# Kernel optimization log

Hardware: AMD Instinct MI355X
Metric: run time of the kernel (lower is better)

Reference implementation:

```python
import jax, jax.numpy as jnp
import numpy as np

H = 16       # query heads
KV = 4       # kv heads
BASE = 10000.0


def _rope(seq_len, head_dim, dtype):
    inv_freq = 1.0 / (BASE ** (jnp.arange(0, head_dim, 2, dtype=jnp.float32) / head_dim))
    t = jnp.arange(seq_len, dtype=jnp.float32)
    freqs = jnp.einsum('i,j->ij', t, inv_freq)          # [S, D/2]
    emb = jnp.concatenate([freqs, freqs], axis=-1)      # [S, D]
    return jnp.cos(emb).astype(dtype), jnp.sin(emb).astype(dtype)


def _rotate_half(x):
    x1, x2 = jnp.split(x, 2, axis=-1)
    return jnp.concatenate([-x2, x1], axis=-1)


def setup_inputs() -> dict:
    key = jax.random.key(0)
    ks = jax.random.split(key, 5)
    B, S, E = 2, 2048, 1024
    return {
        'x': jax.random.normal(ks[0], (B, S, E), jnp.float32),
        'wq': jax.random.normal(ks[1], (E, E), jnp.float32) * (E ** -0.5),
        'wk': jax.random.normal(ks[2], (KV * (E // H), E), jnp.float32) * (E ** -0.5),
        'wv': jax.random.normal(ks[3], (KV * (E // H), E), jnp.float32) * (E ** -0.5),
        'wo': jax.random.normal(ks[4], (E, E), jnp.float32) * (E ** -0.5),
    }


def reference(x, wq, wk, wv, wo):
    B, S, E = x.shape
    D = E // H
    G = H // KV  # query heads per kv head
    scale = D ** -0.5

    q = (x @ wq.T).reshape(B, S, H, D).transpose(0, 2, 1, 3)    # [B,H,S,D]
    k = (x @ wk.T).reshape(B, S, KV, D).transpose(0, 2, 1, 3)   # [B,KV,S,D]
    v = (x @ wv.T).reshape(B, S, KV, D).transpose(0, 2, 1, 3)   # [B,KV,S,D]

    cos, sin = _rope(S, D, x.dtype)                              # [S,D] each
    q = q * cos + _rotate_half(q) * sin
    k = k * cos + _rotate_half(k) * sin

    # GQA: group query heads per kv head instead of materializing repeated K/V
    qg = q.reshape(B, KV, G, S, D)
    scores = jnp.einsum('bkgsd,bktd->bkgst', qg, k) * scale      # [B,KV,G,S,S]
    causal = jnp.triu(jnp.ones((S, S), dtype=bool), k=1)
    scores = jnp.where(causal, jnp.finfo(scores.dtype).min, scores)
    attn = jax.nn.softmax(scores, axis=-1)
    out = jnp.einsum('bkgst,bktd->bkgsd', attn, v)               # [B,KV,G,S,D]
    out = out.reshape(B, H, S, D).transpose(0, 2, 1, 3).reshape(B, S, E)
    return out @ wo.T
```

## Files before the change

### kernel.cpp

```cpp
#include <hip/hip_runtime.h>
#include <stdint.h>

typedef unsigned short u16;
typedef __attribute__((ext_vector_type(8))) short s16x8;
typedef __attribute__((ext_vector_type(4))) float f32x4;
typedef __attribute__((ext_vector_type(4))) unsigned short u16x4;


__device__ __forceinline__ u16 f2bf(float f) {
  unsigned u = __float_as_uint(f);
  unsigned r = (u + 0x7fffu + ((u >> 16) & 1u)) >> 16;
  return (u16)r;
}
__device__ __forceinline__ unsigned pack2(float a, float b) {
  return (unsigned)f2bf(a) | ((unsigned)f2bf(b) << 16);
}
__device__ __forceinline__ float exp2fast(float x) {
  return __builtin_amdgcn_exp2f(x);
}

typedef const __attribute__((address_space(1))) unsigned int* gas_ptr;
typedef __attribute__((address_space(3))) unsigned int* las_ptr;

__device__ __forceinline__ void g2l16(const void* g, void* l) {
  __builtin_amdgcn_global_load_lds((gas_ptr)g, (las_ptr)l, 16, 0, 0);
}

__device__ __forceinline__ void cvt4(const float* __restrict__ in, u16* __restrict__ out) {
  const f32x4 v = *(const f32x4*)in;
  u16x4 o;
  o[0] = f2bf(v[0]); o[1] = f2bf(v[1]); o[2] = f2bf(v[2]); o[3] = f2bf(v[3]);
  *(u16x4*)out = o;
}


__global__ void prep_kernel(const float* __restrict__ x,  const float* __restrict__ wq,
                            const float* __restrict__ wk, const float* __restrict__ wv,
                            const float* __restrict__ wo,
                            u16* __restrict__ xb, u16* __restrict__ wcat, u16* __restrict__ wob,
                            float* __restrict__ cosT, float* __restrict__ sinT) {
  const long id = (long)blockIdx.x * 256 + threadIdx.x;
  if (id < 262144) {
    cvt4(wq + id * 4, wcat + id * 4);
  } else if (id < 327680) {
    const long i = id - 262144;
    cvt4(wk + i * 4, wcat + 1048576 + i * 4);
  } else if (id < 393216) {
    const long i = id - 327680;
    cvt4(wv + i * 4, wcat + 1310720 + i * 4);
  } else if (id < 655360) {
    const long i = id - 393216;
    cvt4(wo + i * 4, wob + i * 4);
  } else if (id < 671744) {
    const long t = id - 655360;
#pragma unroll
    for (int u = 0; u < 4; ++u) {
      const long idx = t * 4 + u;
      const int s = (int)(idx >> 5), j = (int)(idx & 31);
      const double invd = exp(-(double)j * 0.2878231366242558);
      const float a = (float)s * (float)invd;
      cosT[idx] = cosf(a);
      sinT[idx] = sinf(a);
    }
  } else {
    const long i = id - 671744;
    cvt4(x + i * 4, xb + i * 4);
  }
}


__global__ __launch_bounds__(256, 2) void gemm_qkv_kernel(
    const u16* __restrict__ A, const u16* __restrict__ W,
    u16* __restrict__ qo, u16* __restrict__ ko, u16* __restrict__ vto,
    const float* __restrict__ cosT, const float* __restrict__ sinT) {
  const int K = 1024;
  __shared__ __align__(16) u16 As[128 * 32];
  __shared__ __align__(16) u16 Bs[128 * 32];
  const int tid = threadIdx.x;
  const int lane = tid & 63;
  const int wave = tid >> 6;
  const int wr = wave >> 1, wc = wave & 1;
  const long arow0 = (long)blockIdx.x * 128;
  const long wrow0 = (long)blockIdx.y * 128;
  const u16* Ab = A + arow0 * K;
  const u16* Wb = W + wrow0 * K;

  f32x4 acc[4][4] = {};

  for (int k0 = 0; k0 < K; k0 += 32) {
    __syncthreads();
#pragma unroll
    for (int i = 0; i < 2; ++i) {
      const int c = wave * 128 + i * 64 + lane;
      const int r = c >> 2, c16 = c & 3;
      g2l16(Ab + (long)r * K + k0 + c16 * 8, (char*)As + (wave * 128 + i * 64) * 16);
      g2l16(Wb + (long)r * K + k0 + c16 * 8, (char*)Bs + (wave * 128 + i * 64) * 16);
    }
    __syncthreads();
    s16x8 af[4], bfr[4];
#pragma unroll
    for (int m = 0; m < 4; ++m) {
      const int row = wr * 64 + m * 16 + (lane & 15);
      af[m] = *(const s16x8*)&As[row * 32 + (lane >> 4) * 8];
    }
#pragma unroll
    for (int n = 0; n < 4; ++n) {
      const int row = wc * 64 + n * 16 + (lane & 15);
      bfr[n] = *(const s16x8*)&Bs[row * 32 + (lane >> 4) * 8];
    }
    __builtin_amdgcn_s_setprio(1);
#pragma unroll
    for (int m = 0; m < 4; ++m)
#pragma unroll
      for (int n = 0; n < 4; ++n)
        acc[m][n] = __builtin_amdgcn_mfma_f32_16x16x32_bf16(af[m], bfr[n], acc[m][n], 0, 0, 0);
    __builtin_amdgcn_s_setprio(0);
  }

  const int colBase = (int)wrow0 + wc * 64;
  const int j0 = lane & 15;
  const float QSCALE = 0.18033688011112042f;

  if (colBase < 1024) {
    const int h2 = colBase >> 6;
#pragma unroll
    for (int m = 0; m < 4; ++m) {
      const int grow = (int)arow0 + wr * 64 + m * 16 + (lane >> 4) * 4;
#pragma unroll
      for (int r = 0; r < 4; ++r) {
        const int row = grow + r;
        const int s = row & 2047, bb = row >> 11;
        const long ob = (((long)(bb * 16 + h2)) * 2048 + s) * 64;
        const float c0 = cosT[s * 32 + j0],      s0 = sinT[s * 32 + j0];
        const float c1 = cosT[s * 32 + 16 + j0], s1 = sinT[s * 32 + 16 + j0];
        qo[ob + j0]      = f2bf((acc[m][0][r] * c0 - acc[m][2][r] * s0) * QSCALE);
        qo[ob + 16 + j0] = f2bf((acc[m][1][r] * c1 - acc[m][3][r] * s1) * QSCALE);
        qo[ob + 32 + j0] = f2bf((acc[m][2][r] * c0 + acc[m][0][r] * s0) * QSCALE);
        qo[ob + 48 + j0] = f2bf((acc[m][3][r] * c1 + acc[m][1][r] * s1) * QSCALE);
      }
    }
  } else if (colBase < 1280) {
    const int kvh2 = (colBase - 1024) >> 6;
#pragma unroll
    for (int m = 0; m < 4; ++m) {
      const int grow = (int)arow0 + wr * 64 + m * 16 + (lane >> 4) * 4;
#pragma unroll
      for (int r = 0; r < 4; ++r) {
        const int row = grow + r;
        const int s = row & 2047, bb = row >> 11;
        const long ob = (((long)(bb * 4 + kvh2)) * 2048 + s) * 64;
        const float c0 = cosT[s * 32 + j0],      s0 = sinT[s * 32 + j0];
        const float c1 = cosT[s * 32 + 16 + j0], s1 = sinT[s * 32 + 16 + j0];
        ko[ob + j0]      = f2bf(acc[m][0][r] * c0 - acc[m][2][r] * s0);
        ko[ob + 16 + j0] = f2bf(acc[m][1][r] * c1 - acc[m][3][r] * s1);
        ko[ob + 32 + j0] = f2bf(acc[m][2][r] * c0 + acc[m][0][r] * s0);
        ko[ob + 48 + j0] = f2bf(acc[m][3][r] * c1 + acc[m][1][r] * s1);
      }
    }
  } else {
    const int kvh2 = (colBase - 1280) >> 6;
#pragma unroll
    for (int m = 0; m < 4; ++m) {
      const int grow = (int)arow0 + wr * 64 + m * 16 + (lane >> 4) * 4;
#pragma unroll
      for (int r = 0; r < 4; ++r) {
        const int row = grow + r;
        const int s = row & 2047, bb = row >> 11;
#pragma unroll
        for (int n = 0; n < 4; ++n) {
          const int d = n * 16 + j0;
          vto[(((long)(bb * 4 + kvh2)) * 64 + d) * 2048 + s] = f2bf(acc[m][n][r]);
        }
      }
    }
  }
}


__global__ __launch_bounds__(256, 2) void gemm_out_kernel(
    const u16* __restrict__ A, const u16* __restrict__ W, float* __restrict__ Y) {
  const int K = 1024, N = 1024;
  __shared__ __align__(16) u16 As[128 * 32];
  __shared__ __align__(16) u16 Bs[128 * 32];
  const int tid = threadIdx.x;
  const int lane = tid & 63;
  const int wave = tid >> 6;
  const int wr = wave >> 1, wc = wave & 1;
  const long arow0 = (long)blockIdx.x * 128;
  const long wrow0 = (long)blockIdx.y * 128;
  const u16* Ab = A + arow0 * K;
  const u16* Wb = W + wrow0 * K;

  f32x4 acc[4][4] = {};

  for (int k0 = 0; k0 < K; k0 += 32) {
    __syncthreads();
#pragma unroll
    for (int i = 0; i < 2; ++i) {
      const int c = wave * 128 + i * 64 + lane;
      const int r = c >> 2, c16 = c & 3;
      g2l16(Ab + (long)r * K + k0 + c16 * 8, (char*)As + (wave * 128 + i * 64) * 16);
      g2l16(Wb + (long)r * K + k0 + c16 * 8, (char*)Bs + (wave * 128 + i * 64) * 16);
    }
    __syncthreads();
    s16x8 af[4], bfr[4];
#pragma unroll
    for (int m = 0; m < 4; ++m) {
      const int row = wr * 64 + m * 16 + (lane & 15);
      af[m] = *(const s16x8*)&As[row * 32 + (lane >> 4) * 8];
    }
#pragma unroll
    for (int n = 0; n < 4; ++n) {
      const int row = wc * 64 + n * 16 + (lane & 15);
      bfr[n] = *(const s16x8*)&Bs[row * 32 + (lane >> 4) * 8];
    }
    __builtin_amdgcn_s_setprio(1);
#pragma unroll
    for (int m = 0; m < 4; ++m)
#pragma unroll
      for (int n = 0; n < 4; ++n)
        acc[m][n] = __builtin_amdgcn_mfma_f32_16x16x32_bf16(af[m], bfr[n], acc[m][n], 0, 0, 0);
    __builtin_amdgcn_s_setprio(0);
  }

#pragma unroll
  for (int m = 0; m < 4; ++m)
#pragma unroll
    for (int n = 0; n < 4; ++n) {
      const long gr0 = arow0 + wr * 64 + m * 16 + (lane >> 4) * 4;
      const long gc = wrow0 + wc * 64 + n * 16 + (lane & 15);
#pragma unroll
      for (int r = 0; r < 4; ++r)
        Y[(gr0 + r) * N + gc] = acc[m][n][r];
    }
}


__global__ __launch_bounds__(256, 2) void flash_kernel(
    const u16* __restrict__ qg,
    const u16* __restrict__ kg,
    const u16* __restrict__ vtg,
    u16* __restrict__ og) {
  const int tid = threadIdx.x, lane = tid & 63, w = tid >> 6;
  const int g = lane >> 4, l15 = lane & 15;

  const int bid = blockIdx.x;
  const int lid = (bid & 7) * 64 + (bid >> 3);
  const int pr = lid & 15, h = (lid >> 4) & 15, b = lid >> 8;
  const int kvh = h >> 2;

  __shared__ __align__(16) u16 Kl[2][64 * 64];
  __shared__ __align__(16) u16 Vl[2][64 * 64];
  __shared__ __align__(16) u16 Pl[4][16 * 64];

  const u16* Kp = kg  + ((long)(b * 4 + kvh)) * 2048 * 64;
  const u16* Vp = vtg + ((long)(b * 4 + kvh)) * 64 * 2048;

  auto STAGE = [&](int buf, int kt) {
#pragma unroll
    for (int j = 0; j < 2; ++j) {
      const int lbase = j * 256 + w * 64;
      const int c = lbase + lane;
      const int row = c >> 3, c8 = c & 7;
      const int cs = (c8 ^ (row & 7)) * 8;
      g2l16(Kp + ((long)(kt * 64 + row)) * 64 + cs, (char*)Kl[buf] + lbase * 16);
      g2l16(Vp + (long)row * 2048 + kt * 64 + cs,  (char*)Vl[buf] + lbase * 16);
    }
  };

#pragma unroll 1
  for (int pass = 0; pass < 2; ++pass) {
    const int qt = pass ? (31 - pr) : pr;
    const u16* Qp = qg + (((long)(b * 16 + h)) * 2048 + qt * 64 + w * 16) * 64;
    const s16x8 qf0 = *(const s16x8*)(Qp + l15 * 64 + g * 8);
    const s16x8 qf1 = *(const s16x8*)(Qp + l15 * 64 + 32 + g * 8);

    f32x4 of[4] = {};
    float m = -1e30f, lsum = 0.f;
    const int qrow = qt * 64 + w * 16 + l15;

    int cur = 0;
    STAGE(0, 0);

#pragma unroll 1
    for (int kt = 0; kt <= qt; ++kt) {
      if (kt < qt) {
        STAGE(cur ^ 1, kt + 1);
        asm volatile("s_waitcnt vmcnt(4)" ::: "memory");
      } else {
        asm volatile("s_waitcnt vmcnt(0)" ::: "memory");
      }
      __builtin_amdgcn_s_barrier();
      __builtin_amdgcn_sched_barrier(0);
      const u16* Kb = Kl[cur];
      const u16* Vb = Vl[cur];

      f32x4 sf[4] = {};
      __builtin_amdgcn_s_setprio(1);
#pragma unroll
      for (int ks = 0; ks < 2; ++ks) {
        const s16x8 qv = ks ? qf1 : qf0;
#pragma unroll
        for (int fn = 0; fn < 4; ++fn) {
          const int row = fn * 16 + l15;
          const s16x8 kf = *(const s16x8*)((const char*)Kb + row * 128 + (((ks * 4 + g) ^ (row & 7)) << 4));
          sf[fn] = __builtin_amdgcn_mfma_f32_16x16x32_bf16(kf, qv, sf[fn], 0, 0, 0);
        }
      }
      __builtin_amdgcn_s_setprio(0);

      const bool diag = (kt == qt);
      float p[16];
      float mx = -1e30f;
#pragma unroll
      for (int fn = 0; fn < 4; ++fn)
#pragma unroll
        for (int r = 0; r < 4; ++r) {
          float sv = sf[fn][r];
          if (diag) {
            const int kv = kt * 64 + fn * 16 + 4 * g + r;
            if (kv > qrow) sv = -1e30f;
          }
          p[fn * 4 + r] = sv;
          mx = fmaxf(mx, sv);
        }
      mx = fmaxf(mx, __shfl_xor(mx, 16));
      mx = fmaxf(mx, __shfl_xor(mx, 32));

      if (!__all(mx - m <= 11.0f)) {
        const float mn = fmaxf(m, mx);
        const float al = exp2fast(m - mn);
        m = mn;
        lsum *= al;
        float alq[4];
#pragma unroll
        for (int r = 0; r < 4; ++r) alq[r] = __shfl(al, 4 * g + r);
#pragma unroll
        for (int fd = 0; fd < 4; ++fd)
#pragma unroll
          for (int r = 0; r < 4; ++r) of[fd][r] *= alq[r];
      }

      float rs = 0.f;
#pragma unroll
      for (int i = 0; i < 16; ++i) {
        p[i] = exp2fast(p[i] - m);
        rs += p[i];
      }
      rs += __shfl_xor(rs, 16);
      rs += __shfl_xor(rs, 32);
      lsum += rs;

#pragma unroll
      for (int fn = 0; fn < 4; ++fn) {
        const int base = fn * 32 + g * 8;
        char* addr = (char*)Pl[w] + l15 * 128 + ((((base >> 4) ^ (l15 & 7)) << 4) | (base & 15));
        *(unsigned*)addr       = pack2(p[fn * 4 + 0], p[fn * 4 + 1]);
        *(unsigned*)(addr + 4) = pack2(p[fn * 4 + 2], p[fn * 4 + 3]);
      }

      __builtin_amdgcn_s_setprio(1);
#pragma unroll
      for (int ks = 0; ks < 2; ++ks) {
        const s16x8 pa = *(const s16x8*)((const char*)Pl[w] + l15 * 128 + ((((ks * 4 + g)) ^ (l15 & 7)) << 4));
#pragma unroll
        for (int fd = 0; fd < 4; ++fd) {
          const int vrow = fd * 16 + l15;
          const s16x8 vf = *(const s16x8*)((const char*)Vb + vrow * 128 + (((ks * 4 + g) ^ (vrow & 7)) << 4));
          of[fd] = __builtin_amdgcn_mfma_f32_16x16x32_bf16(pa, vf, of[fd], 0, 0, 0);
        }
      }
      __builtin_amdgcn_s_setprio(0);

      __builtin_amdgcn_s_barrier();
      cur ^= 1;
    }

    float linv[4];
#pragma unroll
    for (int r = 0; r < 4; ++r) linv[r] = 1.0f / __shfl(lsum, 4 * g + r);
    const long orow0 = (long)b * 2048 + qt * 64 + w * 16 + 4 * g;
#pragma unroll
    for (int r = 0; r < 4; ++r) {
      const long gb = (orow0 + r) * 1024 + h * 64;
#pragma unroll
      for (int fd = 0; fd < 4; ++fd)
        og[gb + fd * 16 + l15] = f2bf(of[fd][r] * linv[r]);
    }
  }
}


extern "C" void kernel_launch(void* const* d_in, const int* in_sizes, int n_in,
                              void* d_out, int out_size, void* d_ws, size_t ws_size,
                              hipStream_t stream) {
  (void)in_sizes; (void)n_in; (void)out_size; (void)ws_size;
  const float* x  = (const float*)d_in[0];
  const float* wq = (const float*)d_in[1];
  const float* wk = (const float*)d_in[2];
  const float* wv = (const float*)d_in[3];
  const float* wo = (const float*)d_in[4];
  float* out = (float*)d_out;

  char* p = (char*)d_ws;
  auto alloc = [&](size_t bytes) { char* r = p; p += (bytes + 255) & ~(size_t)255; return r; };

  u16* xb    = (u16*)alloc(4096ull * 1024 * 2);
  u16* wcat  = (u16*)alloc(1536ull * 1024 * 2);
  u16* wob   = (u16*)alloc(1024ull * 1024 * 2);
  u16* qrb   = (u16*)alloc(4096ull * 1024 * 2);
  u16* krb   = (u16*)alloc(4096ull * 256 * 2);
  u16* vtb   = (u16*)alloc(4096ull * 256 * 2);
  u16* aob   = (u16*)alloc(4096ull * 1024 * 2);
  float* cosT = (float*)alloc(2048ull * 32 * 4);
  float* sinT = (float*)alloc(2048ull * 32 * 4);

  prep_kernel<<<6720, 256, 0, stream>>>(x, wq, wk, wv, wo, xb, wcat, wob, cosT, sinT);

  gemm_qkv_kernel<<<dim3(32, 12), 256, 0, stream>>>(xb, wcat, qrb, krb, vtb, cosT, sinT);

  flash_kernel<<<512, 256, 0, stream>>>(qrb, krb, vtb, aob);

  gemm_out_kernel<<<dim3(32, 8), 256, 0, stream>>>(aob, wob, out);
}
```

Before: 176.9 us.

## Double GEMM K-tile depth, pad P buffer, use packed bf16 convert in attention

Both projection GEMMs now stage 64-wide K slices per barrier pair instead of 32, halving the barrier and sync count per output tile at the cost of doubled LDS per block. The attention kernel replaces the XOR-swizzled P scratch with a padded 72-element row layout and writes P with a hardware packed bf16 conversion instruction and 8-byte stores. It also restructures the max and sum reductions into trees and drops a scheduling barrier. Rounding of P may differ slightly from the manual round-to-nearest-even helper.

```diff
diff --git a/kernel.cpp b/kernel.cpp
--- a/kernel.cpp
+++ b/kernel.cpp
@@ -5,6 +5,7 @@
 typedef __attribute__((ext_vector_type(8))) short s16x8;
 typedef __attribute__((ext_vector_type(4))) float f32x4;
 typedef __attribute__((ext_vector_type(4))) unsigned short u16x4;
+typedef __attribute__((ext_vector_type(2))) unsigned int u32x2;
 
 
 __device__ __forceinline__ u16 f2bf(float f) {
@@ -12,8 +13,10 @@
   unsigned r = (u + 0x7fffu + ((u >> 16) & 1u)) >> 16;
   return (u16)r;
 }
-__device__ __forceinline__ unsigned pack2(float a, float b) {
-  return (unsigned)f2bf(a) | ((unsigned)f2bf(b) << 16);
+__device__ __forceinline__ unsigned cvt_pk(float lo, float hi) {
+  unsigned r;
+  asm("v_cvt_pk_bf16_f32 %0, %1, %2" : "=v"(r) : "v"(lo), "v"(hi));
+  return r;
 }
 __device__ __forceinline__ float exp2fast(float x) {
   return __builtin_amdgcn_exp2f(x);
@@ -74,11 +77,12 @@
     u16* __restrict__ qo, u16* __restrict__ ko, u16* __restrict__ vto,
     const float* __restrict__ cosT, const float* __restrict__ sinT) {
   const int K = 1024;
-  __shared__ __align__(16) u16 As[128 * 32];
-  __shared__ __align__(16) u16 Bs[128 * 32];
+  __shared__ __align__(16) u16 As[128 * 64];
+  __shared__ __align__(16) u16 Bs[128 * 64];
   const int tid = threadIdx.x;
   const int lane = tid & 63;
   const int wave = tid >> 6;
+  const int g = lane >> 4, l15 = lane & 15;
   const int wr = wave >> 1, wc = wave & 1;
   const long arow0 = (long)blockIdx.x * 128;
   const long wrow0 = (long)blockIdx.y * 128;
@@ -87,45 +91,45 @@
 
   f32x4 acc[4][4] = {};
 
-  for (int k0 = 0; k0 < K; k0 += 32) {
+  for (int k0 = 0; k0 < K; k0 += 64) {
     __syncthreads();
 #pragma unroll
-    for (int i = 0; i < 2; ++i) {
-      const int c = wave * 128 + i * 64 + lane;
-      const int r = c >> 2, c16 = c & 3;
-      g2l16(Ab + (long)r * K + k0 + c16 * 8, (char*)As + (wave * 128 + i * 64) * 16);
-      g2l16(Wb + (long)r * K + k0 + c16 * 8, (char*)Bs + (wave * 128 + i * 64) * 16);
+    for (int i = 0; i < 4; ++i) {
+      const int lbase = i * 256 + wave * 64;
+      const int c = lbase + lane;
+      const int r = c >> 3, c8 = c & 7;
+      g2l16(Ab + (long)r * K + k0 + c8 * 8, (char*)As + lbase * 16);
+      g2l16(Wb + (long)r * K + k0 + c8 * 8, (char*)Bs + lbase * 16);
     }
     __syncthreads();
-    s16x8 af[4], bfr[4];
-#pragma unroll
-    for (int m = 0; m < 4; ++m) {
-      const int row = wr * 64 + m * 16 + (lane & 15);
-      af[m] = *(const s16x8*)&As[row * 32 + (lane >> 4) * 8];
-    }
-#pragma unroll
-    for (int n = 0; n < 4; ++n) {
-      const int row = wc * 64 + n * 16 + (lane & 15);
-      bfr[n] = *(const s16x8*)&Bs[row * 32 + (lane >> 4) * 8];
-    }
-    __builtin_amdgcn_s_setprio(1);
-#pragma unroll
-    for (int m = 0; m < 4; ++m)
+#pragma unroll
+    for (int ks = 0; ks < 2; ++ks) {
+      s16x8 af[4], bfr[4];
+#pragma unroll
+      for (int m = 0; m < 4; ++m)
+        af[m] = *(const s16x8*)&As[(wr * 64 + m * 16 + l15) * 64 + ks * 32 + g * 8];
 #pragma unroll
       for (int n = 0; n < 4; ++n)
-        acc[m][n] = __builtin_amdgcn_mfma_f32_16x16x32_bf16(af[m], bfr[n], acc[m][n], 0, 0, 0);
-    __builtin_amdgcn_s_setprio(0);
+        bfr[n] = *(const s16x8*)&Bs[(wc * 64 + n * 16 + l15) * 64 + ks * 32 + g * 8];
+      __builtin_amdgcn_s_setprio(1);
+#pragma unroll
+      for (int m = 0; m < 4; ++m)
+#pragma unroll
+        for (int n = 0; n < 4; ++n)
+          acc[m][n] = __builtin_amdgcn_mfma_f32_16x16x32_bf16(af[m], bfr[n], acc[m][n], 0, 0, 0);
+      __builtin_amdgcn_s_setprio(0);
+    }
   }
 
   const int colBase = (int)wrow0 + wc * 64;
-  const int j0 = lane & 15;
+  const int j0 = l15;
   const float QSCALE = 0.18033688011112042f;
 
   if (colBase < 1024) {
     const int h2 = colBase >> 6;
 #pragma unroll
     for (int m = 0; m < 4; ++m) {
-      const int grow = (int)arow0 + wr * 64 + m * 16 + (lane >> 4) * 4;
+      const int grow = (int)arow0 + wr * 64 + m * 16 + g * 4;
 #pragma unroll
       for (int r = 0; r < 4; ++r) {
         const int row = grow + r;
@@ -143,7 +147,7 @@
     const int kvh2 = (colBase - 1024) >> 6;
 #pragma unroll
     for (int m = 0; m < 4; ++m) {
-      const int grow = (int)arow0 + wr * 64 + m * 16 + (lane >> 4) * 4;
+      const int grow = (int)arow0 + wr * 64 + m * 16 + g * 4;
 #pragma unroll
       for (int r = 0; r < 4; ++r) {
         const int row = grow + r;
@@ -161,7 +165,7 @@
     const int kvh2 = (colBase - 1280) >> 6;
 #pragma unroll
     for (int m = 0; m < 4; ++m) {
-      const int grow = (int)arow0 + wr * 64 + m * 16 + (lane >> 4) * 4;
+      const int grow = (int)arow0 + wr * 64 + m * 16 + g * 4;
 #pragma unroll
       for (int r = 0; r < 4; ++r) {
         const int row = grow + r;
@@ -180,11 +184,12 @@
 __global__ __launch_bounds__(256, 2) void gemm_out_kernel(
     const u16* __restrict__ A, const u16* __restrict__ W, float* __restrict__ Y) {
   const int K = 1024, N = 1024;
-  __shared__ __align__(16) u16 As[128 * 32];
-  __shared__ __align__(16) u16 Bs[128 * 32];
+  __shared__ __align__(16) u16 As[128 * 64];
+  __shared__ __align__(16) u16 Bs[128 * 64];
   const int tid = threadIdx.x;
   const int lane = tid & 63;
   const int wave = tid >> 6;
+  const int g = lane >> 4, l15 = lane & 15;
   const int wr = wave >> 1, wc = wave & 1;
   const long arow0 = (long)blockIdx.x * 128;
   const long wrow0 = (long)blockIdx.y * 128;
@@ -193,42 +198,42 @@
 
   f32x4 acc[4][4] = {};
 
-  for (int k0 = 0; k0 < K; k0 += 32) {
+  for (int k0 = 0; k0 < K; k0 += 64) {
     __syncthreads();
 #pragma unroll
-    for (int i = 0; i < 2; ++i) {
-      const int c = wave * 128 + i * 64 + lane;
-      const int r = c >> 2, c16 = c & 3;
-      g2l16(Ab + (long)r * K + k0 + c16 * 8, (char*)As + (wave * 128 + i * 64) * 16);
-      g2l16(Wb + (long)r * K + k0 + c16 * 8, (char*)Bs + (wave * 128 + i * 64) * 16);
+    for (int i = 0; i < 4; ++i) {
+      const int lbase = i * 256 + wave * 64;
+      const int c = lbase + lane;
+      const int r = c >> 3, c8 = c & 7;
+      g2l16(Ab + (long)r * K + k0 + c8 * 8, (char*)As + lbase * 16);
+      g2l16(Wb + (long)r * K + k0 + c8 * 8, (char*)Bs + lbase * 16);
     }
     __syncthreads();
-    s16x8 af[4], bfr[4];
-#pragma unroll
-    for (int m = 0; m < 4; ++m) {
-      const int row = wr * 64 + m * 16 + (lane & 15);
-      af[m] = *(const s16x8*)&As[row * 32 + (lane >> 4) * 8];
-    }
+#pragma unroll
+    for (int ks = 0; ks < 2; ++ks) {
+      s16x8 af[4], bfr[4];
+#pragma unroll
+      for (int m = 0; m < 4; ++m)
+        af[m] = *(const s16x8*)&As[(wr * 64 + m * 16 + l15) * 64 + ks * 32 + g * 8];
+#pragma unroll
+      for (int n = 0; n < 4; ++n)
+        bfr[n] = *(const s16x8*)&Bs[(wc * 64 + n * 16 + l15) * 64 + ks * 32 + g * 8];
+      __builtin_amdgcn_s_setprio(1);
+#pragma unroll
+      for (int m = 0; m < 4; ++m)
+#pragma unroll
+        for (int n = 0; n < 4; ++n)
+          acc[m][n] = __builtin_amdgcn_mfma_f32_16x16x32_bf16(af[m], bfr[n], acc[m][n], 0, 0, 0);
+      __builtin_amdgcn_s_setprio(0);
+    }
+  }
+
+#pragma unroll
+  for (int m = 0; m < 4; ++m)
 #pragma unroll
     for (int n = 0; n < 4; ++n) {
-      const int row = wc * 64 + n * 16 + (lane & 15);
-      bfr[n] = *(const s16x8*)&Bs[row * 32 + (lane >> 4) * 8];
-    }
-    __builtin_amdgcn_s_setprio(1);
-#pragma unroll
-    for (int m = 0; m < 4; ++m)
-#pragma unroll
-      for (int n = 0; n < 4; ++n)
-        acc[m][n] = __builtin_amdgcn_mfma_f32_16x16x32_bf16(af[m], bfr[n], acc[m][n], 0, 0, 0);
-    __builtin_amdgcn_s_setprio(0);
-  }
-
-#pragma unroll
-  for (int m = 0; m < 4; ++m)
-#pragma unroll
-    for (int n = 0; n < 4; ++n) {
-      const long gr0 = arow0 + wr * 64 + m * 16 + (lane >> 4) * 4;
-      const long gc = wrow0 + wc * 64 + n * 16 + (lane & 15);
+      const long gr0 = arow0 + wr * 64 + m * 16 + g * 4;
+      const long gc = wrow0 + wc * 64 + n * 16 + l15;
 #pragma unroll
       for (int r = 0; r < 4; ++r)
         Y[(gr0 + r) * N + gc] = acc[m][n][r];
@@ -251,7 +256,7 @@
 
   __shared__ __align__(16) u16 Kl[2][64 * 64];
   __shared__ __align__(16) u16 Vl[2][64 * 64];
-  __shared__ __align__(16) u16 Pl[4][16 * 64];
+  __shared__ __align__(16) u16 Pl[4][16][72];
 
   const u16* Kp = kg  + ((long)(b * 4 + kvh)) * 2048 * 64;
   const u16* Vp = vtg + ((long)(b * 4 + kvh)) * 64 * 2048;
@@ -291,7 +296,6 @@
         asm volatile("s_waitcnt vmcnt(0)" ::: "memory");
       }
       __builtin_amdgcn_s_barrier();
-      __builtin_amdgcn_sched_barrier(0);
       const u16* Kb = Kl[cur];
       const u16* Vb = Vl[cur];
 
@@ -311,7 +315,6 @@
 
       const bool diag = (kt == qt);
       float p[16];
-      float mx = -1e30f;
 #pragma unroll
       for (int fn = 0; fn < 4; ++fn)
 #pragma unroll
@@ -322,8 +325,13 @@
             if (kv > qrow) sv = -1e30f;
           }
           p[fn * 4 + r] = sv;
-          mx = fmaxf(mx, sv);
         }
+      const float t0 = fmaxf(fmaxf(p[0], p[1]), p[2]);
+      const float t1 = fmaxf(fmaxf(p[3], p[4]), p[5]);
+      const float t2 = fmaxf(fmaxf(p[6], p[7]), p[8]);
+      const float t3 = fmaxf(fmaxf(p[9], p[10]), p[11]);
+      const float t4 = fmaxf(fmaxf(p[12], p[13]), p[14]);
+      float mx = fmaxf(fmaxf(fmaxf(t0, t1), t2), fmaxf(fmaxf(t3, t4), p[15]));
       mx = fmaxf(mx, __shfl_xor(mx, 16));
       mx = fmaxf(mx, __shfl_xor(mx, 32));
 
@@ -341,28 +349,29 @@
           for (int r = 0; r < 4; ++r) of[fd][r] *= alq[r];
       }
 
-      float rs = 0.f;
-#pragma unroll
-      for (int i = 0; i < 16; ++i) {
-        p[i] = exp2fast(p[i] - m);
-        rs += p[i];
-      }
+#pragma unroll
+      for (int i = 0; i < 16; ++i) p[i] = exp2fast(p[i] - m);
+      const float s0 = (p[0] + p[1]) + (p[2] + p[3]);
+      const float s1 = (p[4] + p[5]) + (p[6] + p[7]);
+      const float s2 = (p[8] + p[9]) + (p[10] + p[11]);
+      const float s3 = (p[12] + p[13]) + (p[14] + p[15]);
+      float rs = (s0 + s1) + (s2 + s3);
       rs += __shfl_xor(rs, 16);
       rs += __shfl_xor(rs, 32);
       lsum += rs;
 
+      u16* Pw = &Pl[w][l15][0];
 #pragma unroll
       for (int fn = 0; fn < 4; ++fn) {
-        const int base = fn * 32 + g * 8;
-        char* addr = (char*)Pl[w] + l15 * 128 + ((((base >> 4) ^ (l15 & 7)) << 4) | (base & 15));
-        *(unsigned*)addr       = pack2(p[fn * 4 + 0], p[fn * 4 + 1]);
-        *(unsigned*)(addr + 4) = pack2(p[fn * 4 + 2], p[fn * 4 + 3]);
+        const u32x2 v2 = {cvt_pk(p[fn * 4 + 0], p[fn * 4 + 1]),
+                          cvt_pk(p[fn * 4 + 2], p[fn * 4 + 3])};
+        *(u32x2*)(Pw + fn * 16 + g * 4) = v2;
       }
 
       __builtin_amdgcn_s_setprio(1);
 #pragma unroll
       for (int ks = 0; ks < 2; ++ks) {
-        const s16x8 pa = *(const s16x8*)((const char*)Pl[w] + l15 * 128 + ((((ks * 4 + g)) ^ (l15 & 7)) << 4));
+        const s16x8 pa = *(const s16x8*)(&Pl[w][l15][ks * 32 + g * 8]);
 #pragma unroll
         for (int fd = 0; fd < 4; ++fd) {
           const int vrow = fd * 16 + l15;
```

Measured after the change: 174.7 us. About the same (-1.3%).
